# Kernel optimization log

Measured on AMD Instinct MI355X. Metric: run time of the kernel, lower is better.

The kernel has to match this reference:

```python
import jax, jax.numpy as jnp
import numpy as np

EMBED_DIM = 768
NUM_HEADS = 12
HEAD_DIM = EMBED_DIM // NUM_HEADS
SCALE = HEAD_DIM ** -0.5


def setup_inputs() -> dict:
    key = jax.random.key(0)
    k_x, k_qkv, k_pw, k_pb = jax.random.split(key, 4)
    B, N, C = 8, 1024, EMBED_DIM
    x = jax.random.normal(k_x, (B, N, C), dtype=jnp.float32)
    # nn.Linear(embed_dim, 3*embed_dim, bias=False): weight [3C, C]
    w_qkv = jax.random.normal(k_qkv, (3 * C, C), dtype=jnp.float32) * (C ** -0.5)
    # nn.Linear(embed_dim, embed_dim): weight [C, C], bias [C]
    w_proj = jax.random.normal(k_pw, (C, C), dtype=jnp.float32) * (C ** -0.5)
    b_proj = jax.random.normal(k_pb, (C,), dtype=jnp.float32) * 0.01
    return {"x": x, "w_qkv": w_qkv, "w_proj": w_proj, "b_proj": b_proj}


def reference(x, w_qkv, w_proj, b_proj):
    B, N, C = x.shape
    H, D = NUM_HEADS, HEAD_DIM
    # qkv projection: [B, N, 3C] -> [3, B, H, N, D]
    qkv = jnp.einsum('bnc,ec->bne', x, w_qkv)
    qkv = qkv.reshape(B, N, 3, H, D).transpose(2, 0, 3, 1, 4)
    q, k, v = qkv[0], qkv[1], qkv[2]
    # explicit attention matrix [B, H, N, N]
    attn = jax.nn.softmax(jnp.einsum('bhnd,bhmd->bhnm', q, k) * SCALE, axis=-1)
    # attn @ v -> [B, N, C]
    out = jnp.einsum('bhnm,bhmd->bhnd', attn, v)
    out = out.transpose(0, 2, 1, 3).reshape(B, N, C)
    out = jnp.einsum('bnc,oc->bno', out, w_proj) + b_proj
    return out, attn
```

## Files before the change

kernel.cpp:

```cpp
#include <hip/hip_runtime.h>

#define B_ 8
#define N_ 1024
#define C_ 768
#define H_ 12
#define D_ 64
#define SCALE_ 0.125f

typedef _Float16 v8h __attribute__((ext_vector_type(8)));
typedef float v4f __attribute__((ext_vector_type(4)));

__device__ __forceinline__ void gload_lds16(const void* g, void* l) {
    __builtin_amdgcn_global_load_lds((const __attribute__((address_space(1))) void*)g,
                                     (__attribute__((address_space(3))) void*)l, 16, 0, 0);
}

__global__ __launch_bounds__(256) void cast_f2h(const float* __restrict__ src,
                                                _Float16* __restrict__ dst, int n8) {
    const int i = blockIdx.x * 256 + threadIdx.x;
    if (i < n8) {
        const v4f a = *(const v4f*)&src[(size_t)i * 8];
        const v4f b = *(const v4f*)&src[(size_t)i * 8 + 4];
        v8h o;
        o[0] = (_Float16)a[0]; o[1] = (_Float16)a[1]; o[2] = (_Float16)a[2]; o[3] = (_Float16)a[3];
        o[4] = (_Float16)b[0]; o[5] = (_Float16)b[1]; o[6] = (_Float16)b[2]; o[7] = (_Float16)b[3];
        *(v8h*)&dst[(size_t)i * 8] = o;
    }
}

__global__ __launch_bounds__(256) void gemm_qkv(const _Float16* __restrict__ X,
                                                const _Float16* __restrict__ W,
                                                _Float16* __restrict__ qh,
                                                _Float16* __restrict__ kh,
                                                _Float16* __restrict__ vth) {
    __shared__ _Float16 As[2 * 128 * 32];
    __shared__ _Float16 Bs[2 * 128 * 32];
    const int t = threadIdx.x;
    const int w = t >> 6, l = t & 63;
    const int q4 = l >> 4, c0 = l & 15;
    const int wm = w & 1, wn = w >> 1;
    const int m0 = blockIdx.x * 128, n0 = blockIdx.y * 128;
    const int sc8 = (t & 3) * 8;
    const int srow = t >> 2;
    v4f acc[4][4] = {};
    #pragma unroll
    for (int i = 0; i < 2; ++i) {
        const int row = i * 64 + srow;
        gload_lds16(&X[(size_t)(m0 + row) * C_ + sc8], &As[(i * 256 + t) * 8]);
        gload_lds16(&W[(size_t)(n0 + row) * C_ + sc8], &Bs[(i * 256 + t) * 8]);
    }
    __syncthreads();
    int cb = 0;
    for (int k0 = 0; k0 < C_; k0 += 32, cb ^= 1) {
        if (k0 + 32 < C_) {
            const int nb = cb ^ 1;
            #pragma unroll
            for (int i = 0; i < 2; ++i) {
                const int row = i * 64 + srow;
                gload_lds16(&X[(size_t)(m0 + row) * C_ + k0 + 32 + sc8],
                            &As[(nb * 512 + i * 256 + t) * 8]);
                gload_lds16(&W[(size_t)(n0 + row) * C_ + k0 + 32 + sc8],
                            &Bs[(nb * 512 + i * 256 + t) * 8]);
            }
        }
        v8h a[4], b[4];
        #pragma unroll
        for (int mi = 0; mi < 4; ++mi)
            a[mi] = *(const v8h*)&As[cb * 4096 + (wm * 64 + mi * 16 + c0) * 32 + q4 * 8];
        #pragma unroll
        for (int ni = 0; ni < 4; ++ni)
            b[ni] = *(const v8h*)&Bs[cb * 4096 + (wn * 64 + ni * 16 + c0) * 32 + q4 * 8];
        #pragma unroll
        for (int mi = 0; mi < 4; ++mi)
            #pragma unroll
            for (int ni = 0; ni < 4; ++ni)
                acc[mi][ni] = __builtin_amdgcn_mfma_f32_16x16x32_f16(a[mi], b[ni], acc[mi][ni], 0, 0, 0);
        __syncthreads();
    }
    const int which = n0 / C_;
    const int nbase = n0 % C_;
    #pragma unroll
    for (int ni = 0; ni < 4; ++ni) {
        const int n = nbase + wn * 64 + ni * 16 + c0;
        const int h = n >> 6, d = n & 63;
        #pragma unroll
        for (int mi = 0; mi < 4; ++mi) {
            #pragma unroll
            for (int r = 0; r < 4; ++r) {
                const int m = m0 + wm * 64 + mi * 16 + q4 * 4 + r;
                const int b = m >> 10, nn = m & 1023;
                const _Float16 val = (_Float16)acc[mi][ni][r];
                if (which == 0)
                    qh[((size_t)(b * H_ + h) * N_ + nn) * D_ + d] = val;
                else if (which == 1)
                    kh[((size_t)(b * H_ + h) * N_ + nn) * D_ + d] = val;
                else
                    vth[((size_t)(b * H_ + h) * D_ + d) * N_ + nn] = val;
            }
        }
    }
}

__global__ __launch_bounds__(512, 4) void attn_fused(const _Float16* __restrict__ qh,
                                                     const _Float16* __restrict__ kh,
                                                     const _Float16* __restrict__ vth,
                                                     float* __restrict__ attn,
                                                     _Float16* __restrict__ oah) {
    __shared__ _Float16 Qs[2 * 32 * 32];
    __shared__ _Float16 Ks[2 * 2 * 64 * 32];
    __shared__ _Float16 Vt[2 * 2 * 64 * 32];
    __shared__ float Ps[2 * 32 * 68];
    __shared__ float redm[128], reds[128];
    const int t = threadIdx.x;
    const int w = t >> 6, l = t & 63;
    const int q4 = l >> 4, c0 = l & 15;
    const int wg = w >> 2, wl = w & 3;
    const int mt = blockIdx.x, bh = blockIdx.y;
    const size_t qkbase = (size_t)bh * N_ * D_;
    const size_t vtbase = (size_t)bh * D_ * N_;
    const int sp  = t >> 8;
    const int srw = (t >> 2) & 63;
    const int sc8 = (t & 3) * 8;

    if (t < 256) {
        const int qp = t >> 7, qr = (t >> 2) & 31;
        gload_lds16(&qh[qkbase + (size_t)(mt * 32 + qr) * D_ + qp * 32 + sc8], &Qs[t * 8]);
    }
    gload_lds16(&kh[qkbase + (size_t)srw * D_ + sp * 32 + sc8], &Ks[t * 8]);
    __syncthreads();

    const v8h a0 = *(const v8h*)&Qs[(wg * 16 + c0) * 32 + q4 * 8];
    const v8h a1 = *(const v8h*)&Qs[1024 + (wg * 16 + c0) * 32 + q4 * 8];

    v4f S[16];
    #pragma unroll
    for (int i = 0; i < 16; ++i) S[i] = (v4f){0.f, 0.f, 0.f, 0.f};

    #pragma unroll
    for (int c = 0; c < 16; ++c) {
        const int kb = c & 1;
        if (c < 15)
            gload_lds16(&kh[qkbase + (size_t)((c + 1) * 64 + srw) * D_ + sp * 32 + sc8],
                        &Ks[(kb ^ 1) * 4096 + t * 8]);
        const int roff = (wl * 16 + c0) * 32 + q4 * 8;
        const v8h b0 = *(const v8h*)&Ks[kb * 4096 + roff];
        const v8h b1 = *(const v8h*)&Ks[kb * 4096 + 2048 + roff];
        S[c] = __builtin_amdgcn_mfma_f32_16x16x32_f16(a0, b0, S[c], 0, 0, 0);
        S[c] = __builtin_amdgcn_mfma_f32_16x16x32_f16(a1, b1, S[c], 0, 0, 0);
        if (c < 15) __syncthreads();
    }

    float mrow[4] = {-1e30f, -1e30f, -1e30f, -1e30f};
    #pragma unroll
    for (int kt = 0; kt < 16; ++kt)
        #pragma unroll
        for (int r = 0; r < 4; ++r) mrow[r] = fmaxf(mrow[r], S[kt][r]);
    #pragma unroll
    for (int r = 0; r < 4; ++r) {
        #pragma unroll
        for (int mask = 8; mask; mask >>= 1)
            mrow[r] = fmaxf(mrow[r], __shfl_xor(mrow[r], mask, 16));
    }
    if (c0 == 0) {
        #pragma unroll
        for (int r = 0; r < 4; ++r) redm[w * 16 + q4 * 4 + r] = mrow[r];
    }
    __syncthreads();
    gload_lds16(&vth[vtbase + (size_t)srw * N_ + sp * 32 + sc8], &Vt[t * 8]);
    #pragma unroll
    for (int r = 0; r < 4; ++r) {
        const int base = wg * 64 + q4 * 4 + r;
        mrow[r] = fmaxf(fmaxf(redm[base], redm[base + 16]),
                        fmaxf(redm[base + 32], redm[base + 48]));
    }
    float srow[4] = {0.f, 0.f, 0.f, 0.f};
    #pragma unroll
    for (int kt = 0; kt < 16; ++kt)
        #pragma unroll
        for (int r = 0; r < 4; ++r) {
            const float e = __expf((S[kt][r] - mrow[r]) * SCALE_);
            S[kt][r] = e;
            srow[r] += e;
        }
    #pragma unroll
    for (int r = 0; r < 4; ++r) {
        #pragma unroll
        for (int mask = 8; mask; mask >>= 1) srow[r] += __shfl_xor(srow[r], mask, 16);
    }
    if (c0 == 0) {
        #pragma unroll
        for (int r = 0; r < 4; ++r) reds[w * 16 + q4 * 4 + r] = srow[r];
    }
    __syncthreads();
    float inv[4];
    #pragma unroll
    for (int r = 0; r < 4; ++r) {
        const int base = wg * 64 + q4 * 4 + r;
        inv[r] = 1.0f / (reds[base] + reds[base + 16] + reds[base + 32] + reds[base + 48]);
    }
    #pragma unroll
    for (int r = 0; r < 4; ++r)
        Ps[(wg * 16 + q4 * 4 + r) * 68 + wl * 16 + c0] = S[0][r] * inv[r];
    __syncthreads();

    v4f O = {0.f, 0.f, 0.f, 0.f};
    const int arow = t >> 4, acol = (t & 15) * 4;
    float* attn_base = &attn[((size_t)bh * N_ + mt * 32 + arow) * N_ + acol];
    #pragma unroll
    for (int s = 0; s < 16; ++s) {
        const int pb = s & 1;
        if (s < 15) {
            const int nb = pb ^ 1;
            #pragma unroll
            for (int r = 0; r < 4; ++r)
                Ps[nb * 2176 + (wg * 16 + q4 * 4 + r) * 68 + wl * 16 + c0] = S[s + 1][r] * inv[r];
            gload_lds16(&vth[vtbase + (size_t)srw * N_ + (s + 1) * 64 + sp * 32 + sc8],
                        &Vt[nb * 4096 + t * 8]);
        }
        {
            const v4f pv = *(const v4f*)&Ps[pb * 2176 + arow * 68 + acol];
            __builtin_nontemporal_store(pv, (v4f*)(attn_base + s * 64));
        }
        #pragma unroll
        for (int kk = 0; kk < 2; ++kk) {
            const float* pp = &Ps[pb * 2176 + (wg * 16 + c0) * 68 + kk * 32 + q4 * 8];
            const v4f p0 = *(const v4f*)pp;
            const v4f p1 = *(const v4f*)(pp + 4);
            v8h af;
            af[0] = (_Float16)p0[0]; af[1] = (_Float16)p0[1];
            af[2] = (_Float16)p0[2]; af[3] = (_Float16)p0[3];
            af[4] = (_Float16)p1[0]; af[5] = (_Float16)p1[1];
            af[6] = (_Float16)p1[2]; af[7] = (_Float16)p1[3];
            const v8h bf = *(const v8h*)&Vt[pb * 4096 + kk * 2048 + (wl * 16 + c0) * 32 + q4 * 8];
            O = __builtin_amdgcn_mfma_f32_16x16x32_f16(af, bf, O, 0, 0, 0);
        }
        if (s < 15) __syncthreads();
    }
    const int b = bh / H_, h = bh % H_;
    #pragma unroll
    for (int r = 0; r < 4; ++r)
        oah[((size_t)b * N_ + mt * 32 + wg * 16 + q4 * 4 + r) * C_ + h * D_ + wl * 16 + c0] =
            (_Float16)O[r];
}

__global__ __launch_bounds__(256) void gemm_proj(const _Float16* __restrict__ X,
                                                 const _Float16* __restrict__ W,
                                                 const float* __restrict__ Bias,
                                                 float* __restrict__ out) {
    __shared__ _Float16 As[2 * 128 * 32];
    __shared__ _Float16 Bs[2 * 128 * 32];
    const int t = threadIdx.x;
    const int w = t >> 6, l = t & 63;
    const int q4 = l >> 4, c0 = l & 15;
    const int wm = w & 1, wn = w >> 1;
    const int m0 = blockIdx.x * 128, n0 = blockIdx.y * 128;
    const int sc8 = (t & 3) * 8;
    const int srow = t >> 2;
    v4f acc[4][4] = {};
    #pragma unroll
    for (int i = 0; i < 2; ++i) {
        const int row = i * 64 + srow;
        gload_lds16(&X[(size_t)(m0 + row) * C_ + sc8], &As[(i * 256 + t) * 8]);
        gload_lds16(&W[(size_t)(n0 + row) * C_ + sc8], &Bs[(i * 256 + t) * 8]);
    }
    __syncthreads();
    int cb = 0;
    for (int k0 = 0; k0 < C_; k0 += 32, cb ^= 1) {
        if (k0 + 32 < C_) {
            const int nb = cb ^ 1;
            #pragma unroll
            for (int i = 0; i < 2; ++i) {
                const int row = i * 64 + srow;
                gload_lds16(&X[(size_t)(m0 + row) * C_ + k0 + 32 + sc8],
                            &As[(nb * 512 + i * 256 + t) * 8]);
                gload_lds16(&W[(size_t)(n0 + row) * C_ + k0 + 32 + sc8],
                            &Bs[(nb * 512 + i * 256 + t) * 8]);
            }
        }
        v8h a[4], b[4];
        #pragma unroll
        for (int mi = 0; mi < 4; ++mi)
            a[mi] = *(const v8h*)&As[cb * 4096 + (wm * 64 + mi * 16 + c0) * 32 + q4 * 8];
        #pragma unroll
        for (int ni = 0; ni < 4; ++ni)
            b[ni] = *(const v8h*)&Bs[cb * 4096 + (wn * 64 + ni * 16 + c0) * 32 + q4 * 8];
        #pragma unroll
        for (int mi = 0; mi < 4; ++mi)
            #pragma unroll
            for (int ni = 0; ni < 4; ++ni)
                acc[mi][ni] = __builtin_amdgcn_mfma_f32_16x16x32_f16(a[mi], b[ni], acc[mi][ni], 0, 0, 0);
        __syncthreads();
    }
    #pragma unroll
    for (int ni = 0; ni < 4; ++ni) {
        const int n = n0 + wn * 64 + ni * 16 + c0;
        const float bias = Bias[n];
        #pragma unroll
        for (int mi = 0; mi < 4; ++mi) {
            #pragma unroll
            for (int r = 0; r < 4; ++r) {
                const int m = m0 + wm * 64 + mi * 16 + q4 * 4 + r;
                __builtin_nontemporal_store(acc[mi][ni][r] + bias, &out[(size_t)m * C_ + n]);
            }
        }
    }
}

extern "C" void kernel_launch(void* const* d_in, const int* in_sizes, int n_in,
                              void* d_out, int out_size, void* d_ws, size_t ws_size,
                              hipStream_t stream) {
    const float* x      = (const float*)d_in[0];
    const float* w_qkv  = (const float*)d_in[1];
    const float* w_proj = (const float*)d_in[2];
    const float* b_proj = (const float*)d_in[3];

    float* out  = (float*)d_out;
    float* attn = out + (size_t)B_ * N_ * C_;

    const size_t NX  = (size_t)B_ * N_ * C_;
    const size_t NWQ = (size_t)3 * C_ * C_;
    const size_t NWP = (size_t)C_ * C_;
    _Float16* xh  = (_Float16*)d_ws;
    _Float16* wqh = xh + NX;
    _Float16* wph = wqh + NWQ;
    _Float16* qh  = wph + NWP;
    _Float16* kh  = qh + NX;
    _Float16* vth = kh + NX;
    _Float16* oah = vth + NX;

    cast_f2h<<<dim3((int)(NX / 8 / 256)), 256, 0, stream>>>(x, xh, (int)(NX / 8));
    cast_f2h<<<dim3((int)(NWQ / 8 / 256)), 256, 0, stream>>>(w_qkv, wqh, (int)(NWQ / 8));
    cast_f2h<<<dim3((int)(NWP / 8 / 256)), 256, 0, stream>>>(w_proj, wph, (int)(NWP / 8));

    gemm_qkv  <<<dim3(64, 18), 256, 0, stream>>>(xh, wqh, qh, kh, vth);
    attn_fused<<<dim3(32, 96), 512, 0, stream>>>(qh, kh, vth, attn, oah);
    gemm_proj <<<dim3(64, 6), 256, 0, stream>>>(oah, wph, b_proj, out);
}
```

Measured before the change: 577.9 us.

## Triple-buffer K/V tiles with fine-grained vmcnt waits in fused attention

```diff
diff --git a/kernel.cpp b/kernel.cpp
--- a/kernel.cpp
+++ b/kernel.cpp
@@ -13,6 +13,16 @@
 __device__ __forceinline__ void gload_lds16(const void* g, void* l) {
     __builtin_amdgcn_global_load_lds((const __attribute__((address_space(1))) void*)g,
                                      (__attribute__((address_space(3))) void*)l, 16, 0, 0);
+}
+
+__device__ __forceinline__ void raw_sync() {
+    __builtin_amdgcn_sched_barrier(0);
+    __builtin_amdgcn_s_barrier();
+    __builtin_amdgcn_sched_barrier(0);
+}
+__device__ __forceinline__ void lgkm0() {
+    asm volatile("s_waitcnt lgkmcnt(0)" ::: "memory");
+    __builtin_amdgcn_sched_barrier(0);
 }
 
 __global__ __launch_bounds__(256) void cast_f2h(const float* __restrict__ src,
@@ -106,9 +116,8 @@
                                                      const _Float16* __restrict__ vth,
                                                      float* __restrict__ attn,
                                                      _Float16* __restrict__ oah) {
-    __shared__ _Float16 Qs[2 * 32 * 32];
-    __shared__ _Float16 Ks[2 * 2 * 64 * 32];
-    __shared__ _Float16 Vt[2 * 2 * 64 * 32];
+    __shared__ _Float16 Ks[3 * 2 * 64 * 32];
+    __shared__ _Float16 Vt[3 * 2 * 64 * 32];
     __shared__ float Ps[2 * 32 * 68];
     __shared__ float redm[128], reds[128];
     const int t = threadIdx.x;
@@ -122,15 +131,12 @@
     const int srw = (t >> 2) & 63;
     const int sc8 = (t & 3) * 8;
 
-    if (t < 256) {
-        const int qp = t >> 7, qr = (t >> 2) & 31;
-        gload_lds16(&qh[qkbase + (size_t)(mt * 32 + qr) * D_ + qp * 32 + sc8], &Qs[t * 8]);
-    }
+    const _Float16* qp = &qh[qkbase + (size_t)(mt * 32 + wg * 16 + c0) * D_ + q4 * 8];
+    const v8h a0 = *(const v8h*)qp;
+    const v8h a1 = *(const v8h*)(qp + 32);
+
     gload_lds16(&kh[qkbase + (size_t)srw * D_ + sp * 32 + sc8], &Ks[t * 8]);
-    __syncthreads();
-
-    const v8h a0 = *(const v8h*)&Qs[(wg * 16 + c0) * 32 + q4 * 8];
-    const v8h a1 = *(const v8h*)&Qs[1024 + (wg * 16 + c0) * 32 + q4 * 8];
+    gload_lds16(&kh[qkbase + (size_t)(64 + srw) * D_ + sp * 32 + sc8], &Ks[4096 + t * 8]);
 
     v4f S[16];
     #pragma unroll
@@ -138,16 +144,19 @@
 
     #pragma unroll
     for (int c = 0; c < 16; ++c) {
-        const int kb = c & 1;
-        if (c < 15)
-            gload_lds16(&kh[qkbase + (size_t)((c + 1) * 64 + srw) * D_ + sp * 32 + sc8],
-                        &Ks[(kb ^ 1) * 4096 + t * 8]);
+        if (c == 15) asm volatile("s_waitcnt vmcnt(0)" ::: "memory");
+        else         asm volatile("s_waitcnt vmcnt(1)" ::: "memory");
+        raw_sync();
+        const int kb = (c % 3) * 4096;
         const int roff = (wl * 16 + c0) * 32 + q4 * 8;
-        const v8h b0 = *(const v8h*)&Ks[kb * 4096 + roff];
-        const v8h b1 = *(const v8h*)&Ks[kb * 4096 + 2048 + roff];
+        const v8h b0 = *(const v8h*)&Ks[kb + roff];
+        const v8h b1 = *(const v8h*)&Ks[kb + 2048 + roff];
         S[c] = __builtin_amdgcn_mfma_f32_16x16x32_f16(a0, b0, S[c], 0, 0, 0);
         S[c] = __builtin_amdgcn_mfma_f32_16x16x32_f16(a1, b1, S[c], 0, 0, 0);
-        if (c < 15) __syncthreads();
+        if (c + 2 < 16)
+            gload_lds16(&kh[qkbase + (size_t)((c + 2) * 64 + srw) * D_ + sp * 32 + sc8],
+                        &Ks[((c + 2) % 3) * 4096 + t * 8]);
+        lgkm0();
     }
 
     float mrow[4] = {-1e30f, -1e30f, -1e30f, -1e30f};
@@ -165,8 +174,10 @@
         #pragma unroll
         for (int r = 0; r < 4; ++r) redm[w * 16 + q4 * 4 + r] = mrow[r];
     }
-    __syncthreads();
+    lgkm0();
+    raw_sync();
     gload_lds16(&vth[vtbase + (size_t)srw * N_ + sp * 32 + sc8], &Vt[t * 8]);
+    gload_lds16(&vth[vtbase + (size_t)srw * N_ + 64 + sp * 32 + sc8], &Vt[4096 + t * 8]);
     #pragma unroll
     for (int r = 0; r < 4; ++r) {
         const int base = wg * 64 + q4 * 4 + r;
@@ -191,7 +202,8 @@
         #pragma unroll
         for (int r = 0; r < 4; ++r) reds[w * 16 + q4 * 4 + r] = srow[r];
     }
-    __syncthreads();
+    lgkm0();
+    raw_sync();
     float inv[4];
     #pragma unroll
     for (int r = 0; r < 4; ++r) {
@@ -201,29 +213,24 @@
     #pragma unroll
     for (int r = 0; r < 4; ++r)
         Ps[(wg * 16 + q4 * 4 + r) * 68 + wl * 16 + c0] = S[0][r] * inv[r];
-    __syncthreads();
+    lgkm0();
 
     v4f O = {0.f, 0.f, 0.f, 0.f};
     const int arow = t >> 4, acol = (t & 15) * 4;
     float* attn_base = &attn[((size_t)bh * N_ + mt * 32 + arow) * N_ + acol];
+    const int afrow = (wg * 16 + c0) * 68;
     #pragma unroll
     for (int s = 0; s < 16; ++s) {
-        const int pb = s & 1;
-        if (s < 15) {
-            const int nb = pb ^ 1;
-            #pragma unroll
-            for (int r = 0; r < 4; ++r)
-                Ps[nb * 2176 + (wg * 16 + q4 * 4 + r) * 68 + wl * 16 + c0] = S[s + 1][r] * inv[r];
-            gload_lds16(&vth[vtbase + (size_t)srw * N_ + (s + 1) * 64 + sp * 32 + sc8],
-                        &Vt[nb * 4096 + t * 8]);
-        }
-        {
-            const v4f pv = *(const v4f*)&Ps[pb * 2176 + arow * 68 + acol];
-            __builtin_nontemporal_store(pv, (v4f*)(attn_base + s * 64));
-        }
+        if (s == 0 || s == 15) asm volatile("s_waitcnt vmcnt(1)" ::: "memory");
+        else                   asm volatile("s_waitcnt vmcnt(2)" ::: "memory");
+        raw_sync();
+        const int pb = (s & 1) * 2176;
+        const v4f pv = *(const v4f*)&Ps[pb + arow * 68 + acol];
+        __builtin_nontemporal_store(pv, (v4f*)(attn_base + s * 64));
+        const int vb = (s % 3) * 4096;
         #pragma unroll
         for (int kk = 0; kk < 2; ++kk) {
-            const float* pp = &Ps[pb * 2176 + (wg * 16 + c0) * 68 + kk * 32 + q4 * 8];
+            const float* pp = &Ps[pb + afrow + kk * 32 + q4 * 8];
             const v4f p0 = *(const v4f*)pp;
             const v4f p1 = *(const v4f*)(pp + 4);
             v8h af;
@@ -231,10 +238,18 @@
             af[2] = (_Float16)p0[2]; af[3] = (_Float16)p0[3];
             af[4] = (_Float16)p1[0]; af[5] = (_Float16)p1[1];
             af[6] = (_Float16)p1[2]; af[7] = (_Float16)p1[3];
-            const v8h bf = *(const v8h*)&Vt[pb * 4096 + kk * 2048 + (wl * 16 + c0) * 32 + q4 * 8];
+            const v8h bf = *(const v8h*)&Vt[vb + kk * 2048 + (wl * 16 + c0) * 32 + q4 * 8];
             O = __builtin_amdgcn_mfma_f32_16x16x32_f16(af, bf, O, 0, 0, 0);
         }
-        if (s < 15) __syncthreads();
+        if (s < 15) {
+            #pragma unroll
+            for (int r = 0; r < 4; ++r)
+                Ps[(pb ^ 2176) + (wg * 16 + q4 * 4 + r) * 68 + wl * 16 + c0] = S[s + 1][r] * inv[r];
+            if (s + 2 < 16)
+                gload_lds16(&vth[vtbase + (size_t)srw * N_ + (s + 2) * 64 + sp * 32 + sc8],
+                            &Vt[((s + 2) % 3) * 4096 + t * 8]);
+        }
+        lgkm0();
     }
     const int b = bh / H_, h = bh % H_;
     #pragma unroll
```

After: 563.5 us. 2.5% less time.

## Load Q/K/V operands directly from global memory and stage full fp16 P row in LDS

Applied to the files above, without the earlier changes.

```diff
diff --git a/kernel.cpp b/kernel.cpp
--- a/kernel.cpp
+++ b/kernel.cpp
@@ -106,10 +106,7 @@
                                                      const _Float16* __restrict__ vth,
                                                      float* __restrict__ attn,
                                                      _Float16* __restrict__ oah) {
-    __shared__ _Float16 Qs[2 * 32 * 32];
-    __shared__ _Float16 Ks[2 * 2 * 64 * 32];
-    __shared__ _Float16 Vt[2 * 2 * 64 * 32];
-    __shared__ float Ps[2 * 32 * 68];
+    __shared__ _Float16 Ph[32 * 1032];
     __shared__ float redm[128], reds[128];
     const int t = threadIdx.x;
     const int w = t >> 6, l = t & 63;
@@ -118,36 +115,22 @@
     const int mt = blockIdx.x, bh = blockIdx.y;
     const size_t qkbase = (size_t)bh * N_ * D_;
     const size_t vtbase = (size_t)bh * D_ * N_;
-    const int sp  = t >> 8;
-    const int srw = (t >> 2) & 63;
-    const int sc8 = (t & 3) * 8;
-
-    if (t < 256) {
-        const int qp = t >> 7, qr = (t >> 2) & 31;
-        gload_lds16(&qh[qkbase + (size_t)(mt * 32 + qr) * D_ + qp * 32 + sc8], &Qs[t * 8]);
-    }
-    gload_lds16(&kh[qkbase + (size_t)srw * D_ + sp * 32 + sc8], &Ks[t * 8]);
-    __syncthreads();
-
-    const v8h a0 = *(const v8h*)&Qs[(wg * 16 + c0) * 32 + q4 * 8];
-    const v8h a1 = *(const v8h*)&Qs[1024 + (wg * 16 + c0) * 32 + q4 * 8];
+
+    const _Float16* qp = &qh[qkbase + (size_t)(mt * 32 + wg * 16 + c0) * D_ + q4 * 8];
+    const v8h a0 = *(const v8h*)qp;
+    const v8h a1 = *(const v8h*)(qp + 32);
 
     v4f S[16];
     #pragma unroll
     for (int i = 0; i < 16; ++i) S[i] = (v4f){0.f, 0.f, 0.f, 0.f};
 
-    #pragma unroll
+    const _Float16* kp = &kh[qkbase + (size_t)(wl * 16 + c0) * D_ + q4 * 8];
+    #pragma unroll 2
     for (int c = 0; c < 16; ++c) {
-        const int kb = c & 1;
-        if (c < 15)
-            gload_lds16(&kh[qkbase + (size_t)((c + 1) * 64 + srw) * D_ + sp * 32 + sc8],
-                        &Ks[(kb ^ 1) * 4096 + t * 8]);
-        const int roff = (wl * 16 + c0) * 32 + q4 * 8;
-        const v8h b0 = *(const v8h*)&Ks[kb * 4096 + roff];
-        const v8h b1 = *(const v8h*)&Ks[kb * 4096 + 2048 + roff];
-        S[c] = __builtin_amdgcn_mfma_f32_16x16x32_f16(a0, b0, S[c], 0, 0, 0);
-        S[c] = __builtin_amdgcn_mfma_f32_16x16x32_f16(a1, b1, S[c], 0, 0, 0);
-        if (c < 15) __syncthreads();
+        const v8h b0 = *(const v8h*)(kp + (size_t)c * 64 * D_);
+        const v8h b1 = *(const v8h*)(kp + (size_t)c * 64 * D_ + 32);
+        const v4f acc = __builtin_amdgcn_mfma_f32_16x16x32_f16(a0, b0, S[c], 0, 0, 0);
+        S[c] = __builtin_amdgcn_mfma_f32_16x16x32_f16(a1, b1, acc, 0, 0, 0);
     }
 
     float mrow[4] = {-1e30f, -1e30f, -1e30f, -1e30f};
@@ -166,7 +149,6 @@
         for (int r = 0; r < 4; ++r) redm[w * 16 + q4 * 4 + r] = mrow[r];
     }
     __syncthreads();
-    gload_lds16(&vth[vtbase + (size_t)srw * N_ + sp * 32 + sc8], &Vt[t * 8]);
     #pragma unroll
     for (int r = 0; r < 4; ++r) {
         const int base = wg * 64 + q4 * 4 + r;
@@ -198,49 +180,38 @@
         const int base = wg * 64 + q4 * 4 + r;
         inv[r] = 1.0f / (reds[base] + reds[base + 16] + reds[base + 32] + reds[base + 48]);
     }
-    #pragma unroll
-    for (int r = 0; r < 4; ++r)
-        Ps[(wg * 16 + q4 * 4 + r) * 68 + wl * 16 + c0] = S[0][r] * inv[r];
-    __syncthreads();
-
-    v4f O = {0.f, 0.f, 0.f, 0.f};
-    const int arow = t >> 4, acol = (t & 15) * 4;
-    float* attn_base = &attn[((size_t)bh * N_ + mt * 32 + arow) * N_ + acol];
-    #pragma unroll
+
+    #pragma unroll
+    for (int r = 0; r < 4; ++r) {
+        const int row = wg * 16 + q4 * 4 + r;
+        float* ab = &attn[((size_t)bh * N_ + mt * 32 + row) * N_ + wl * 16 + c0];
+        _Float16* pb = &Ph[row * 1032 + wl * 16 + c0];
+        #pragma unroll
+        for (int kt = 0; kt < 16; ++kt) {
+            const float p = S[kt][r] * inv[r];
+            __builtin_nontemporal_store(p, ab + kt * 64);
+            pb[kt * 64] = (_Float16)p;
+        }
+    }
+    __syncthreads();
+
+    v4f O0 = {0.f, 0.f, 0.f, 0.f}, O1 = {0.f, 0.f, 0.f, 0.f};
+    const _Float16* vp = &vth[vtbase + (size_t)(wl * 16 + c0) * N_ + q4 * 8];
+    const _Float16* pf = &Ph[(wg * 16 + c0) * 1032 + q4 * 8];
+    #pragma unroll 2
     for (int s = 0; s < 16; ++s) {
-        const int pb = s & 1;
-        if (s < 15) {
-            const int nb = pb ^ 1;
-            #pragma unroll
-            for (int r = 0; r < 4; ++r)
-                Ps[nb * 2176 + (wg * 16 + q4 * 4 + r) * 68 + wl * 16 + c0] = S[s + 1][r] * inv[r];
-            gload_lds16(&vth[vtbase + (size_t)srw * N_ + (s + 1) * 64 + sp * 32 + sc8],
-                        &Vt[nb * 4096 + t * 8]);
-        }
-        {
-            const v4f pv = *(const v4f*)&Ps[pb * 2176 + arow * 68 + acol];
-            __builtin_nontemporal_store(pv, (v4f*)(attn_base + s * 64));
-        }
-        #pragma unroll
-        for (int kk = 0; kk < 2; ++kk) {
-            const float* pp = &Ps[pb * 2176 + (wg * 16 + c0) * 68 + kk * 32 + q4 * 8];
-            const v4f p0 = *(const v4f*)pp;
-            const v4f p1 = *(const v4f*)(pp + 4);
-            v8h af;
-            af[0] = (_Float16)p0[0]; af[1] = (_Float16)p0[1];
-            af[2] = (_Float16)p0[2]; af[3] = (_Float16)p0[3];
-            af[4] = (_Float16)p1[0]; af[5] = (_Float16)p1[1];
-            af[6] = (_Float16)p1[2]; af[7] = (_Float16)p1[3];
-            const v8h bf = *(const v8h*)&Vt[pb * 4096 + kk * 2048 + (wl * 16 + c0) * 32 + q4 * 8];
-            O = __builtin_amdgcn_mfma_f32_16x16x32_f16(af, bf, O, 0, 0, 0);
-        }
-        if (s < 15) __syncthreads();
+        const v8h af0 = *(const v8h*)(pf + s * 64);
+        const v8h bf0 = *(const v8h*)(vp + s * 64);
+        const v8h af1 = *(const v8h*)(pf + s * 64 + 32);
+        const v8h bf1 = *(const v8h*)(vp + s * 64 + 32);
+        O0 = __builtin_amdgcn_mfma_f32_16x16x32_f16(af0, bf0, O0, 0, 0, 0);
+        O1 = __builtin_amdgcn_mfma_f32_16x16x32_f16(af1, bf1, O1, 0, 0, 0);
     }
     const int b = bh / H_, h = bh % H_;
     #pragma unroll
     for (int r = 0; r < 4; ++r)
         oah[((size_t)b * N_ + mt * 32 + wg * 16 + q4 * 4 + r) * C_ + h * D_ + wl * 16 + c0] =
-            (_Float16)O[r];
+            (_Float16)(O0[r] + O1[r]);
 }
 
 __global__ __launch_bounds__(256) void gemm_proj(const _Float16* __restrict__ X,
```

Measured after the change: 1.042 ms. 80.4% more time.
